# Kernel optimization log

Measured on AMD Instinct MI355X. Metric: run time of the kernel, lower is better.

## Reference

```python
import jax, jax.numpy as jnp
import numpy as np

N_NODES = 50000      # nodes
N_EDGES = 800000     # edges (avg degree 16)
D = 128              # input_dim == hidden_dim
C = 32               # output_dim (classes)
G = 64               # number of graphs in batch
EPS = 1e-5           # LayerNorm eps (torch default)
NUM_LAYERS = 3


def setup_inputs() -> dict:
    key = jax.random.key(0)
    ks = jax.random.split(key, 12)
    scale = 1.0 / np.sqrt(D)
    x = jax.random.normal(ks[0], (N_NODES, D), dtype=jnp.float32)
    edge_index = jax.random.randint(ks[1], (2, N_EDGES), 0, N_NODES)
    batch = jnp.sort(jax.random.randint(ks[2], (N_NODES,), 0, G))
    # CustomConv params: self-loop linear + message linear, 3 layers stacked
    W_self = jax.random.normal(ks[3], (NUM_LAYERS, D, D), dtype=jnp.float32) * scale
    b_self = jnp.zeros((NUM_LAYERS, D), dtype=jnp.float32)
    W_msg = jax.random.normal(ks[4], (NUM_LAYERS, D, D), dtype=jnp.float32) * scale
    b_msg = jnp.zeros((NUM_LAYERS, D), dtype=jnp.float32)
    # two LayerNorms (after layers 0 and 1)
    ln_g = jnp.ones((2, D), dtype=jnp.float32)
    ln_b = jnp.zeros((2, D), dtype=jnp.float32)
    # post-MP MLP head: Linear(D,D) -> Dropout(identity in eval) -> Linear(D,C)
    W1 = jax.random.normal(ks[5], (D, D), dtype=jnp.float32) * scale
    b1 = jnp.zeros((D,), dtype=jnp.float32)
    W2 = jax.random.normal(ks[6], (D, C), dtype=jnp.float32) * scale
    b2 = jnp.zeros((C,), dtype=jnp.float32)
    return {"x": x, "W_self": W_self, "b_self": b_self, "W_msg": W_msg,
            "b_msg": b_msg, "ln_g": ln_g, "ln_b": ln_b, "W1": W1, "b1": b1,
            "W2": W2, "b2": b2, "edge_index": edge_index, "batch": batch}


def _layer_norm(h, g, b):
    mu = jnp.mean(h, axis=-1, keepdims=True)
    var = jnp.mean(jnp.square(h - mu), axis=-1, keepdims=True)
    return g * (h - mu) * jax.lax.rsqrt(var + EPS) + b


def reference(x, W_self, b_self, W_msg, b_msg, ln_g, ln_b, W1, b1, W2, b2,
              edge_index, batch):
    src, dst = edge_index[0], edge_index[1]
    for i in range(NUM_LAYERS):
        # CustomConv: self linear + sum-aggregated neighbor messages
        msg = x @ W_msg[i] + b_msg[i]                     # [N, D]
        agg = jax.ops.segment_sum(msg[src], dst, num_segments=N_NODES)
        x = x @ W_self[i] + b_self[i] + agg               # [N, D]
        x = jax.nn.relu(x)
        # dropout p=0.25 is identity in eval mode
        if i != NUM_LAYERS - 1:
            x = _layer_norm(x, ln_g[i], ln_b[i])
    # global mean pool over graphs
    sums = jax.ops.segment_sum(x, batch, num_segments=G)          # [G, D]
    cnt = jax.ops.segment_sum(jnp.ones((N_NODES,), x.dtype), batch,
                              num_segments=G)                     # [G]
    pooled = sums / jnp.maximum(cnt, 1.0)[:, None]
    # post-MP head (dropout identity in eval)
    h = pooled @ W1 + b1
    logits = h @ W2 + b2                                          # [G, C]
    return jax.nn.log_softmax(logits, axis=1)
```

## Files before the change

kernel.cpp:

```cpp
#include <hip/hip_runtime.h>
#include <hip/hip_bf16.h>
#include <math.h>

#define N_NODES 50000
#define N_EDGES 800000
#define DIM 128
#define CLS 32
#define NGRAPH 64
#define LN_EPS 1e-5f
#define CSR_CAP (N_EDGES + 8 * N_NODES)
#define NBLK ((N_NODES + 255) / 256)
#define EPB (N_EDGES / 256)
#define EB_STRIDE 5120
#define LCAP 8192
#define PSPLIT 16

typedef __attribute__((ext_vector_type(8))) short bf16x8;
typedef __attribute__((ext_vector_type(4))) float f32x4;

static __device__ __forceinline__ int lower_bound_i(const int* a, int n, int key) {
    int lo = 0, hi = n;
    while (lo < hi) { int mid = (lo + hi) >> 1; if (a[mid] < key) lo = mid + 1; else hi = mid; }
    return lo;
}


__global__ __launch_bounds__(256) void prep_kernel(
    const float* __restrict__ x, const float* __restrict__ Wself,
    const float* __restrict__ Wmsg, __hip_bfloat16* __restrict__ XbIn,
    __hip_bfloat16* __restrict__ WT, int* __restrict__ counts,
    int* __restrict__ ecur, float* __restrict__ gsum,
    __hip_bfloat16* __restrict__ padA, __hip_bfloat16* __restrict__ padB,
    __hip_bfloat16* __restrict__ padC, __hip_bfloat16* __restrict__ padD) {
    int i = blockIdx.x * 256 + threadIdx.x;
    if (i < N_NODES * DIM / 2) {
        float2 v = ((const float2*)x)[i];
        ((__hip_bfloat162*)XbIn)[i] = __float22bfloat162_rn(v);
    }
    if (i < 3 * 128 * 256) {
        int l = i / (128 * 256);
        int rem = i - l * (128 * 256);
        int n = rem >> 8;
        int k = rem & 255;
        float v = (k < 128) ? Wself[l * 16384 + k * 128 + n]
                            : Wmsg[l * 16384 + (k - 128) * 128 + n];
        WT[i] = __float2bfloat16(v);
    }
    if (i < N_NODES) counts[i] = 0;
    if (i < NBLK) ecur[i] = i * EB_STRIDE;
    if (i < NGRAPH * DIM) gsum[i] = 0.f;
    if (i < DIM) {
        padA[i] = __float2bfloat16(0.f);
        padB[i] = __float2bfloat16(0.f);
        padC[i] = __float2bfloat16(0.f);
        padD[i] = __float2bfloat16(0.f);
    }
}


__global__ __launch_bounds__(1024) void bucket_kernel(
    const int* __restrict__ esrc, const int* __restrict__ edst,
    int* __restrict__ cnt, int* __restrict__ ecur, int* __restrict__ ebuf) {
    __shared__ int bc[NBLK];
    const int t = threadIdx.x;
    const int e0 = blockIdx.x * EPB;
    if (t < NBLK) bc[t] = 0;
    __syncthreads();
    for (int i = t; i < EPB; i += 1024) {
        int d = edst[e0 + i];
        atomicAdd(&cnt[d], 1);
        atomicAdd(&bc[d >> 8], 1);
    }
    __syncthreads();
    if (t < NBLK) {
        int c = bc[t];
        bc[t] = atomicAdd(&ecur[t], c);
    }
    __syncthreads();
    for (int i = t; i < EPB; i += 1024) {
        int d = edst[e0 + i];
        int s = esrc[e0 + i];
        int pos = atomicAdd(&bc[d >> 8], 1);
        ebuf[pos] = ((d & 255) << 16) | s;
    }
}


__global__ __launch_bounds__(256) void scan_part1_kernel(const int* __restrict__ cnt,
                                                         int* __restrict__ bsum) {
    __shared__ int sd[256];
    int gi = blockIdx.x * 256 + threadIdx.x;
    int v = (gi < N_NODES) ? ((cnt[gi] + 7) & ~7) : 0;
    sd[threadIdx.x] = v;
    __syncthreads();
    for (int o = 128; o > 0; o >>= 1) {
        if (threadIdx.x < o) sd[threadIdx.x] += sd[threadIdx.x + o];
        __syncthreads();
    }
    if (threadIdx.x == 0) bsum[blockIdx.x] = sd[0];
}

__global__ __launch_bounds__(256) void scan_part2_kernel(int* __restrict__ bsum) {
    __shared__ int sd[256];
    int i = threadIdx.x;
    int v = (i < NBLK) ? bsum[i] : 0;
    sd[i] = v;
    __syncthreads();
    for (int o = 1; o < 256; o <<= 1) {
        int t = (i >= o) ? sd[i - o] : 0;
        __syncthreads();
        sd[i] += t;
        __syncthreads();
    }
    if (i < NBLK) bsum[i] = sd[i] - v;
}

__global__ __launch_bounds__(256) void scan_part3_kernel(const int* __restrict__ cnt,
                                                         const int* __restrict__ bsum,
                                                         int* __restrict__ off) {
    __shared__ int sd[256];
    int gi = blockIdx.x * 256 + threadIdx.x;
    int i = threadIdx.x;
    int c = (gi < N_NODES) ? cnt[gi] : 0;
    int v = (c + 7) & ~7;
    sd[i] = v;
    __syncthreads();
    for (int o = 1; o < 256; o <<= 1) {
        int t = (i >= o) ? sd[i - o] : 0;
        __syncthreads();
        sd[i] += t;
        __syncthreads();
    }
    int incl = sd[i];
    int base = bsum[blockIdx.x];
    if (gi < N_NODES) off[gi] = base + incl - v;
    if (gi == N_NODES - 1) off[N_NODES] = base + incl;
}


__global__ __launch_bounds__(1024) void csr_build_kernel(
    const int* __restrict__ ebuf, const int* __restrict__ ecur,
    const int* __restrict__ bsum, int* __restrict__ csr) {
    __shared__ int ncnt[256];
    __shared__ int ssc[256];
    __shared__ int lcsr[LCAP];
    const int b = blockIdx.x;
    const int t = threadIdx.x;
    const int bsize = ecur[b] - b * EB_STRIDE;
    const int* eb = ebuf + b * EB_STRIDE;
    for (int i = t; i < LCAP; i += 1024) lcsr[i] = N_NODES;
    if (t < 256) ncnt[t] = 0;
    __syncthreads();
    for (int i = t; i < bsize; i += 1024) atomicAdd(&ncnt[eb[i] >> 16], 1);
    __syncthreads();
    int mypad = 0;
    if (t < 256) { mypad = (ncnt[t] + 7) & ~7; ssc[t] = mypad; }
    __syncthreads();
    for (int o = 1; o < 256; o <<= 1) {
        int v = 0;
        if (t < 256 && t >= o) v = ssc[t - o];
        __syncthreads();
        if (t < 256) ssc[t] += v;
        __syncthreads();
    }
    if (t < 256) ncnt[t] = ssc[t] - mypad;
    __syncthreads();
    for (int i = t; i < bsize; i += 1024) {
        int p = eb[i];
        int pos = atomicAdd(&ncnt[p >> 16], 1);
        if (pos < LCAP) lcsr[pos] = p & 0xFFFF;
    }
    __syncthreads();
    const int total = ssc[255];
    const int gbase = bsum[b];
    int4* dst4 = (int4*)(csr + gbase);
    const int4* src4 = (const int4*)lcsr;
    for (int i = t; i < (total >> 2); i += 1024) dst4[i] = src4[i];
}


__global__ __launch_bounds__(256) void agg_kernel(const __hip_bfloat16* __restrict__ Xb,
                                                  const int* __restrict__ off,
                                                  const int* __restrict__ csr,
                                                  __hip_bfloat16* __restrict__ Sb) {
    int wave = threadIdx.x >> 6;
    int lane = threadIdx.x & 63;
    int n = blockIdx.x * 4 + wave;
    if (n >= N_NODES) return;
    int b = off[n], e = off[n + 1];
    float ax = 0.f, ay = 0.f;
    const size_t coloff = (size_t)(lane * 2);
    int base = b;
    for (; base + 16 <= e; base += 16) {
        int idx16 = csr[base + (lane & 15)];
        int s[16];
        unsigned int v[16];
#pragma unroll
        for (int j = 0; j < 16; j++) s[j] = __shfl(idx16, j, 64);
#pragma unroll
        for (int j = 0; j < 16; j++)
            v[j] = *(const unsigned int*)(Xb + (size_t)s[j] * DIM + coloff);
#pragma unroll
        for (int j = 0; j < 16; j++) {
            union { unsigned int u; float f; } lo, hi;
            lo.u = v[j] << 16;
            hi.u = v[j] & 0xffff0000u;
            ax += lo.f;
            ay += hi.f;
        }
    }
    if (base < e) {
        int idx8 = csr[base + (lane & 7)];
        int s[8];
        unsigned int v[8];
#pragma unroll
        for (int j = 0; j < 8; j++) s[j] = __shfl(idx8, j, 64);
#pragma unroll
        for (int j = 0; j < 8; j++)
            v[j] = *(const unsigned int*)(Xb + (size_t)s[j] * DIM + coloff);
#pragma unroll
        for (int j = 0; j < 8; j++) {
            union { unsigned int u; float f; } lo, hi;
            lo.u = v[j] << 16;
            hi.u = v[j] & 0xffff0000u;
            ax += lo.f;
            ay += hi.f;
        }
    }
    ((__hip_bfloat162*)(Sb + (size_t)n * DIM))[lane] =
        __float22bfloat162_rn(make_float2(ax, ay));
}


__global__ __launch_bounds__(256) void layer_mfma_kernel(
    const __hip_bfloat16* __restrict__ Xb, const __hip_bfloat16* __restrict__ Sb,
    const __hip_bfloat16* __restrict__ WT,
    const float* __restrict__ bself, const float* __restrict__ bmsg,
    const int* __restrict__ deg,
    const float* __restrict__ lng, const float* __restrict__ lnb,
    __hip_bfloat16* __restrict__ XoutB, int do_ln) {
    __shared__ __hip_bfloat16 wlds[128 * 136];
    const int tid = threadIdx.x;
    const int w = tid >> 6, lane = tid & 63;
    const int l15 = lane & 15, q = lane >> 4;

    const int row = blockIdx.x * 64 + w * 16 + l15;
    const int rowc = min(row, N_NODES);

    f32x4 acc[8];
#pragma unroll
    for (int ct = 0; ct < 8; ct++) acc[ct] = (f32x4){0.f, 0.f, 0.f, 0.f};

    const __hip_bfloat16* Abase[2] = {Xb, Sb};
    for (int c = 0; c < 2; c++) {
        __syncthreads();
        {
            int n = tid >> 1, h = tid & 1;
            const uint4* src = (const uint4*)(WT + n * 256 + c * 128 + h * 64);
            uint4* dst = (uint4*)(&wlds[n * 136 + h * 64]);
#pragma unroll
            for (int i = 0; i < 8; i++) dst[i] = src[i];
        }
        __syncthreads();
        const __hip_bfloat16* arow = Abase[c] + (size_t)rowc * DIM;
#pragma unroll
        for (int ks = 0; ks < 4; ks++) {
            bf16x8 afrag = *(const bf16x8*)(arow + ks * 32 + q * 8);
#pragma unroll
            for (int ct = 0; ct < 8; ct++) {
                bf16x8 bfrag = *(const bf16x8*)(&wlds[(ct * 16 + l15) * 136 + ks * 32 + q * 8]);
                acc[ct] = __builtin_amdgcn_mfma_f32_16x16x32_bf16(afrag, bfrag, acc[ct], 0, 0, 0);
            }
        }
    }

    const int growbase = blockIdx.x * 64 + w * 16;
#pragma unroll
    for (int r = 0; r < 4; r++) {
        int grow = growbase + q * 4 + r;
        bool valid = grow < N_NODES;
        float dg = valid ? (float)deg[grow] : 0.f;
        float v[8];
        float s1 = 0.f;
#pragma unroll
        for (int ct = 0; ct < 8; ct++) {
            int col = ct * 16 + l15;
            float h = acc[ct][r] + bself[col] + dg * bmsg[col];
            h = fmaxf(h, 0.f);
            v[ct] = h;
            s1 += h;
        }
        if (do_ln) {
#pragma unroll
            for (int m = 1; m < 16; m <<= 1) s1 += __shfl_xor(s1, m, 64);
            float mu = s1 * (1.0f / 128.0f);
            float s2 = 0.f;
#pragma unroll
            for (int ct = 0; ct < 8; ct++) { float d = v[ct] - mu; s2 += d * d; }
#pragma unroll
            for (int m = 1; m < 16; m <<= 1) s2 += __shfl_xor(s2, m, 64);
            float rs = rsqrtf(s2 * (1.0f / 128.0f) + LN_EPS);
#pragma unroll
            for (int ct = 0; ct < 8; ct++) {
                int col = ct * 16 + l15;
                v[ct] = lng[col] * (v[ct] - mu) * rs + lnb[col];
            }
        }
        if (valid) {
#pragma unroll
            for (int ct = 0; ct < 8; ct++) {
                int col = ct * 16 + l15;
                XoutB[(size_t)grow * DIM + col] = __float2bfloat16(v[ct]);
            }
        }
    }
}


__global__ __launch_bounds__(128) void pool_partial_kernel(const __hip_bfloat16* __restrict__ X,
                                                           const int* __restrict__ batch,
                                                           float* __restrict__ gsum) {
    int g = blockIdx.x;
    int s = blockIdx.y;
    int lo = lower_bound_i(batch, N_NODES, g);
    int hi = lower_bound_i(batch, N_NODES, g + 1);
    int len = hi - lo;
    int a = lo + (int)(((long long)len * s) / PSPLIT);
    int b = lo + (int)(((long long)len * (s + 1)) / PSPLIT);
    int c = threadIdx.x;
    float acc = 0.f;
    for (int n = a; n < b; n++) acc += __bfloat162float(X[(size_t)n * DIM + c]);
    if (b > a) atomicAdd(&gsum[g * DIM + c], acc);
}

__global__ __launch_bounds__(128) void head_kernel(
    const float* __restrict__ gsum, const int* __restrict__ batch,
    const float* __restrict__ W1, const float* __restrict__ b1,
    const float* __restrict__ W2, const float* __restrict__ b2,
    float* __restrict__ out) {
    __shared__ float p[128];
    __shared__ float hh[128];
    int g = blockIdx.x;
    int j = threadIdx.x;
    int lo = lower_bound_i(batch, N_NODES, g);
    int hi = lower_bound_i(batch, N_NODES, g + 1);
    float cnt = fmaxf((float)(hi - lo), 1.0f);
    p[j] = gsum[g * DIM + j] / cnt;
    __syncthreads();
    float s = b1[j];
    for (int k = 0; k < DIM; k++) s += p[k] * W1[k * DIM + j];
    hh[j] = s;
    __syncthreads();
    if (j < CLS) {
        float l = b2[j];
        for (int k = 0; k < DIM; k++) l += hh[k] * W2[k * CLS + j];
        float mx = l;
#pragma unroll
        for (int m = 16; m >= 1; m >>= 1) mx = fmaxf(mx, __shfl_xor(mx, m, 64));
        float ex = expf(l - mx);
        float se = ex;
#pragma unroll
        for (int m = 16; m >= 1; m >>= 1) se += __shfl_xor(se, m, 64);
        out[g * CLS + j] = l - mx - logf(se);
    }
}


extern "C" void kernel_launch(void* const* d_in, const int* in_sizes, int n_in,
                              void* d_out, int out_size, void* d_ws, size_t ws_size,
                              hipStream_t stream) {
    (void)in_sizes; (void)n_in; (void)out_size; (void)ws_size;
    const float* x     = (const float*)d_in[0];
    const float* Wself = (const float*)d_in[1];
    const float* bself = (const float*)d_in[2];
    const float* Wmsg  = (const float*)d_in[3];
    const float* bmsg  = (const float*)d_in[4];
    const float* lng   = (const float*)d_in[5];
    const float* lnb   = (const float*)d_in[6];
    const float* W1    = (const float*)d_in[7];
    const float* b1    = (const float*)d_in[8];
    const float* W2    = (const float*)d_in[9];
    const float* b2    = (const float*)d_in[10];
    const int*   ei    = (const int*)d_in[11];
    const int*   batch = (const int*)d_in[12];
    const int* esrc = ei;
    const int* edst = ei + N_EDGES;

    char* w = (char*)d_ws;
    size_t o = 0;
    auto alloc = [&](size_t bytes) { void* p = w + o; o += (bytes + 255) & ~(size_t)255; return p; };
    __hip_bfloat16* XbIn = (__hip_bfloat16*)alloc((size_t)(N_NODES + 1) * DIM * 2);
    __hip_bfloat16* Xb0  = (__hip_bfloat16*)alloc((size_t)(N_NODES + 1) * DIM * 2);
    __hip_bfloat16* Xb1  = (__hip_bfloat16*)alloc((size_t)(N_NODES + 1) * DIM * 2);
    __hip_bfloat16* Sb   = (__hip_bfloat16*)alloc((size_t)(N_NODES + 1) * DIM * 2);
    __hip_bfloat16* WT   = (__hip_bfloat16*)alloc((size_t)3 * 128 * 256 * 2);
    int*   counts = (int*)alloc((size_t)N_NODES * 4);
    int*   offs   = (int*)alloc((size_t)(N_NODES + 1) * 4);
    int*   bsum   = (int*)alloc((size_t)NBLK * 4);
    int*   ecur   = (int*)alloc((size_t)NBLK * 4);
    int*   ebuf   = (int*)alloc((size_t)NBLK * EB_STRIDE * 4);
    int*   csr    = (int*)alloc((size_t)CSR_CAP * 4);
    float* gsum   = (float*)alloc((size_t)NGRAPH * DIM * 4);

    prep_kernel<<<(N_NODES * DIM / 2 + 255) / 256, 256, 0, stream>>>(
        x, Wself, Wmsg, XbIn, WT, counts, ecur, gsum,
        XbIn + (size_t)N_NODES * DIM, Xb0 + (size_t)N_NODES * DIM,
        Xb1 + (size_t)N_NODES * DIM, Sb + (size_t)N_NODES * DIM);

    bucket_kernel<<<256, 1024, 0, stream>>>(esrc, edst, counts, ecur, ebuf);
    scan_part1_kernel<<<NBLK, 256, 0, stream>>>(counts, bsum);
    scan_part2_kernel<<<1, 256, 0, stream>>>(bsum);
    scan_part3_kernel<<<NBLK, 256, 0, stream>>>(counts, bsum, offs);
    csr_build_kernel<<<NBLK, 1024, 0, stream>>>(ebuf, ecur, bsum, csr);

    const __hip_bfloat16* XbCur = XbIn;
    __hip_bfloat16* bbufs[3] = {Xb0, Xb1, Xb0};
    for (int i = 0; i < 3; i++) {
        agg_kernel<<<(N_NODES + 3) / 4, 256, 0, stream>>>(XbCur, offs, csr, Sb);
        layer_mfma_kernel<<<(N_NODES + 63) / 64, 256, 0, stream>>>(
            XbCur, Sb, WT + (size_t)i * 128 * 256,
            bself + i * DIM, bmsg + i * DIM, counts,
            (i < 2) ? lng + i * DIM : lng, (i < 2) ? lnb + i * DIM : lnb,
            bbufs[i], (i < 2) ? 1 : 0);
        XbCur = bbufs[i];
    }

    pool_partial_kernel<<<dim3(NGRAPH, PSPLIT), 128, 0, stream>>>(bbufs[2], batch, gsum);
    head_kernel<<<NGRAPH, 128, 0, stream>>>(gsum, batch, W1, b1, W2, b2, (float*)d_out);
}
```

Before: 324.0 us.

## Replace global per-node atomics and 3-pass scan with per-bucket histograms

Removes the per-edge global atomicAdd on node counts in the bucket kernel. Per-node counts are now computed inside a new per-bucket histogram kernel using shared-memory atomics. The three-kernel prefix scan becomes a single small scan over bucket totals, and per-node offsets are written in csr_build. Bucket reservations are padded to 16 with -1 sentinels, and the bucketing grid is halved to 128 blocks, trading an extra pass over ebuf for fewer launches and less global atomic contention.

```diff
diff --git a/kernel.cpp b/kernel.cpp
--- a/kernel.cpp
+++ b/kernel.cpp
@@ -9,9 +9,10 @@
 #define NGRAPH 64
 #define LN_EPS 1e-5f
 #define CSR_CAP (N_EDGES + 8 * N_NODES)
-#define NBLK ((N_NODES + 255) / 256)
-#define EPB (N_EDGES / 256)
-#define EB_STRIDE 5120
+#define NBLK 196
+#define ABLK 128
+#define EPB (N_EDGES / ABLK)
+#define EB_STRIDE 7168
 #define LCAP 8192
 #define PSPLIT 16
 
@@ -28,7 +29,7 @@
 __global__ __launch_bounds__(256) void prep_kernel(
     const float* __restrict__ x, const float* __restrict__ Wself,
     const float* __restrict__ Wmsg, __hip_bfloat16* __restrict__ XbIn,
-    __hip_bfloat16* __restrict__ WT, int* __restrict__ counts,
+    __hip_bfloat16* __restrict__ WT,
     int* __restrict__ ecur, float* __restrict__ gsum,
     __hip_bfloat16* __restrict__ padA, __hip_bfloat16* __restrict__ padB,
     __hip_bfloat16* __restrict__ padC, __hip_bfloat16* __restrict__ padD) {
@@ -46,7 +47,6 @@
                             : Wmsg[l * 16384 + (k - 128) * 128 + n];
         WT[i] = __float2bfloat16(v);
     }
-    if (i < N_NODES) counts[i] = 0;
     if (i < NBLK) ecur[i] = i * EB_STRIDE;
     if (i < NGRAPH * DIM) gsum[i] = 0.f;
     if (i < DIM) {
@@ -60,21 +60,22 @@
 
 __global__ __launch_bounds__(1024) void bucket_kernel(
     const int* __restrict__ esrc, const int* __restrict__ edst,
-    int* __restrict__ cnt, int* __restrict__ ecur, int* __restrict__ ebuf) {
-    __shared__ int bc[NBLK];
+    int* __restrict__ ecur, int* __restrict__ ebuf) {
+    __shared__ int bc[NBLK], bres[NBLK], bcnt[NBLK];
     const int t = threadIdx.x;
     const int e0 = blockIdx.x * EPB;
     if (t < NBLK) bc[t] = 0;
     __syncthreads();
-    for (int i = t; i < EPB; i += 1024) {
-        int d = edst[e0 + i];
-        atomicAdd(&cnt[d], 1);
-        atomicAdd(&bc[d >> 8], 1);
-    }
+    for (int i = t; i < EPB; i += 1024)
+        atomicAdd(&bc[edst[e0 + i] >> 8], 1);
     __syncthreads();
     if (t < NBLK) {
         int c = bc[t];
-        bc[t] = atomicAdd(&ecur[t], c);
+        int r = (c + 15) & ~15;
+        int res = atomicAdd(&ecur[t], r);
+        bres[t] = res;
+        bcnt[t] = c;
+        bc[t] = res;
     }
     __syncthreads();
     for (int i = t; i < EPB; i += 1024) {
@@ -83,78 +84,81 @@
         int pos = atomicAdd(&bc[d >> 8], 1);
         ebuf[pos] = ((d & 255) << 16) | s;
     }
-}
-
-
-__global__ __launch_bounds__(256) void scan_part1_kernel(const int* __restrict__ cnt,
-                                                         int* __restrict__ bsum) {
-    __shared__ int sd[256];
-    int gi = blockIdx.x * 256 + threadIdx.x;
-    int v = (gi < N_NODES) ? ((cnt[gi] + 7) & ~7) : 0;
-    sd[threadIdx.x] = v;
+    __syncthreads();
+    if (t < NBLK) {
+        int c = bcnt[t], r = (c + 15) & ~15, base = bres[t];
+        for (int j = c; j < r; j++) ebuf[base + j] = -1;
+    }
+}
+
+
+__global__ __launch_bounds__(1024) void bhist_kernel(
+    const int* __restrict__ ebuf, const int* __restrict__ ecur,
+    int* __restrict__ counts, int* __restrict__ btot) {
+    __shared__ int ncnt[256];
+    __shared__ int red[256];
+    const int b = blockIdx.x, t = threadIdx.x;
+    const int used = ecur[b] - b * EB_STRIDE;
+    const int* eb = ebuf + b * EB_STRIDE;
+    if (t < 256) ncnt[t] = 0;
+    __syncthreads();
+    for (int i = t; i < used; i += 1024) {
+        int p = eb[i];
+        if (p != -1) atomicAdd(&ncnt[p >> 16], 1);
+    }
+    __syncthreads();
+    if (t < 256) {
+        int gi = b * 256 + t;
+        if (gi < N_NODES) counts[gi] = ncnt[t];
+        red[t] = (ncnt[t] + 7) & ~7;
+    }
     __syncthreads();
     for (int o = 128; o > 0; o >>= 1) {
-        if (threadIdx.x < o) sd[threadIdx.x] += sd[threadIdx.x + o];
-        __syncthreads();
-    }
-    if (threadIdx.x == 0) bsum[blockIdx.x] = sd[0];
-}
-
-__global__ __launch_bounds__(256) void scan_part2_kernel(int* __restrict__ bsum) {
+        if (t < o) red[t] += red[t + o];
+        __syncthreads();
+    }
+    if (t == 0) btot[b] = red[0];
+}
+
+
+__global__ __launch_bounds__(256) void btot_scan_kernel(const int* __restrict__ btot,
+                                                        int* __restrict__ bbase,
+                                                        int* __restrict__ off) {
     __shared__ int sd[256];
     int i = threadIdx.x;
-    int v = (i < NBLK) ? bsum[i] : 0;
+    int v = (i < NBLK) ? btot[i] : 0;
     sd[i] = v;
     __syncthreads();
     for (int o = 1; o < 256; o <<= 1) {
-        int t = (i >= o) ? sd[i - o] : 0;
-        __syncthreads();
-        sd[i] += t;
-        __syncthreads();
-    }
-    if (i < NBLK) bsum[i] = sd[i] - v;
-}
-
-__global__ __launch_bounds__(256) void scan_part3_kernel(const int* __restrict__ cnt,
-                                                         const int* __restrict__ bsum,
-                                                         int* __restrict__ off) {
-    __shared__ int sd[256];
-    int gi = blockIdx.x * 256 + threadIdx.x;
-    int i = threadIdx.x;
-    int c = (gi < N_NODES) ? cnt[gi] : 0;
-    int v = (c + 7) & ~7;
-    sd[i] = v;
-    __syncthreads();
-    for (int o = 1; o < 256; o <<= 1) {
-        int t = (i >= o) ? sd[i - o] : 0;
-        __syncthreads();
-        sd[i] += t;
-        __syncthreads();
-    }
-    int incl = sd[i];
-    int base = bsum[blockIdx.x];
-    if (gi < N_NODES) off[gi] = base + incl - v;
-    if (gi == N_NODES - 1) off[N_NODES] = base + incl;
+        int tv = (i >= o) ? sd[i - o] : 0;
+        __syncthreads();
+        sd[i] += tv;
+        __syncthreads();
+    }
+    if (i < NBLK) bbase[i] = sd[i] - v;
+    if (i == 255) off[N_NODES] = sd[255];
 }
 
 
 __global__ __launch_bounds__(1024) void csr_build_kernel(
     const int* __restrict__ ebuf, const int* __restrict__ ecur,
-    const int* __restrict__ bsum, int* __restrict__ csr) {
-    __shared__ int ncnt[256];
+    const int* __restrict__ counts, const int* __restrict__ bbase,
+    int* __restrict__ off, int* __restrict__ csr) {
+    __shared__ int cur[256];
     __shared__ int ssc[256];
     __shared__ int lcsr[LCAP];
-    const int b = blockIdx.x;
-    const int t = threadIdx.x;
-    const int bsize = ecur[b] - b * EB_STRIDE;
+    const int b = blockIdx.x, t = threadIdx.x;
+    const int used = ecur[b] - b * EB_STRIDE;
     const int* eb = ebuf + b * EB_STRIDE;
+    const int gbase = bbase[b];
     for (int i = t; i < LCAP; i += 1024) lcsr[i] = N_NODES;
-    if (t < 256) ncnt[t] = 0;
-    __syncthreads();
-    for (int i = t; i < bsize; i += 1024) atomicAdd(&ncnt[eb[i] >> 16], 1);
-    __syncthreads();
-    int mypad = 0;
-    if (t < 256) { mypad = (ncnt[t] + 7) & ~7; ssc[t] = mypad; }
+    int myc = 0, mypad = 0;
+    const int gi = b * 256 + t;
+    if (t < 256) {
+        myc = (gi < N_NODES) ? counts[gi] : 0;
+        mypad = (myc + 7) & ~7;
+        ssc[t] = mypad;
+    }
     __syncthreads();
     for (int o = 1; o < 256; o <<= 1) {
         int v = 0;
@@ -163,16 +167,21 @@
         if (t < 256) ssc[t] += v;
         __syncthreads();
     }
-    if (t < 256) ncnt[t] = ssc[t] - mypad;
-    __syncthreads();
-    for (int i = t; i < bsize; i += 1024) {
+    if (t < 256) {
+        int eoff = ssc[t] - mypad;
+        cur[t] = eoff;
+        if (gi < N_NODES) off[gi] = gbase + eoff;
+    }
+    __syncthreads();
+    for (int i = t; i < used; i += 1024) {
         int p = eb[i];
-        int pos = atomicAdd(&ncnt[p >> 16], 1);
-        if (pos < LCAP) lcsr[pos] = p & 0xFFFF;
+        if (p != -1) {
+            int pos = atomicAdd(&cur[p >> 16], 1);
+            lcsr[pos] = p & 0xFFFF;
+        }
     }
     __syncthreads();
     const int total = ssc[255];
-    const int gbase = bsum[b];
     int4* dst4 = (int4*)(csr + gbase);
     const int4* src4 = (const int4*)lcsr;
     for (int i = t; i < (total >> 2); i += 1024) dst4[i] = src4[i];
@@ -396,22 +405,22 @@
     __hip_bfloat16* WT   = (__hip_bfloat16*)alloc((size_t)3 * 128 * 256 * 2);
     int*   counts = (int*)alloc((size_t)N_NODES * 4);
     int*   offs   = (int*)alloc((size_t)(N_NODES + 1) * 4);
-    int*   bsum   = (int*)alloc((size_t)NBLK * 4);
+    int*   btot   = (int*)alloc((size_t)NBLK * 4);
+    int*   bbase  = (int*)alloc((size_t)NBLK * 4);
     int*   ecur   = (int*)alloc((size_t)NBLK * 4);
     int*   ebuf   = (int*)alloc((size_t)NBLK * EB_STRIDE * 4);
     int*   csr    = (int*)alloc((size_t)CSR_CAP * 4);
     float* gsum   = (float*)alloc((size_t)NGRAPH * DIM * 4);
 
     prep_kernel<<<(N_NODES * DIM / 2 + 255) / 256, 256, 0, stream>>>(
-        x, Wself, Wmsg, XbIn, WT, counts, ecur, gsum,
+        x, Wself, Wmsg, XbIn, WT, ecur, gsum,
         XbIn + (size_t)N_NODES * DIM, Xb0 + (size_t)N_NODES * DIM,
         Xb1 + (size_t)N_NODES * DIM, Sb + (size_t)N_NODES * DIM);
 
-    bucket_kernel<<<256, 1024, 0, stream>>>(esrc, edst, counts, ecur, ebuf);
-    scan_part1_kernel<<<NBLK, 256, 0, stream>>>(counts, bsum);
-    scan_part2_kernel<<<1, 256, 0, stream>>>(bsum);
-    scan_part3_kernel<<<NBLK, 256, 0, stream>>>(counts, bsum, offs);
-    csr_build_kernel<<<NBLK, 1024, 0, stream>>>(ebuf, ecur, bsum, csr);
+    bucket_kernel<<<ABLK, 1024, 0, stream>>>(esrc, edst, ecur, ebuf);
+    bhist_kernel<<<NBLK, 1024, 0, stream>>>(ebuf, ecur, counts, btot);
+    btot_scan_kernel<<<1, 256, 0, stream>>>(btot, bbase, offs);
+    csr_build_kernel<<<NBLK, 1024, 0, stream>>>(ebuf, ecur, counts, bbase, offs, csr);
 
     const __hip_bfloat16* XbCur = XbIn;
     __hip_bfloat16* bbufs[3] = {Xb0, Xb1, Xb0};
```

Result: faster. 294.5 us (-9.1%).
